# Kernel optimization log

Hardware: AMD Instinct MI355X
Metric: run time of the kernel (lower is better)

The kernel has to match this reference:

```python
import jax, jax.numpy as jnp
import numpy as np

DIM_D = 32
DIM_J = 32
DIM_X = 2 * DIM_D + 1  # 65: (dim_d+1) vd slice + dim_d C_R slice
DIM_H = 256
N = 100
DT = 0.01
JUMP_P = 0.05  # per-step jump probability
BATCH = 4096


def setup_inputs() -> dict:
    key = jax.random.key(0)
    ks = jax.random.split(key, 8)

    def he(k, shape):  # kaiming_normal_, fan_in mode (matches torch init)
        return (jax.random.normal(k, shape, dtype=jnp.float32)
                * jnp.sqrt(2.0 / shape[1]))

    W1 = he(ks[0], (DIM_H, DIM_X + 1))
    W2 = he(ks[1], (DIM_H, DIM_H))
    W3 = he(ks[2], (DIM_H, DIM_H))
    W4 = he(ks[3], (DIM_D, DIM_H))
    b1 = jnp.zeros((DIM_H,), jnp.float32)
    b2 = jnp.zeros((DIM_H,), jnp.float32)
    b3 = jnp.zeros((DIM_H,), jnp.float32)
    b4 = jnp.zeros((DIM_D,), jnp.float32)
    # x_0 in (0, 0.5) so -log(1 - x) is well defined; s, d positive rates
    x_0 = jax.random.uniform(ks[4], (DIM_X,), jnp.float32, 0.05, 0.5)
    s = jax.random.uniform(ks[5], (DIM_D, 1), jnp.float32, 0.5, 1.5)
    d_param = jax.random.uniform(ks[6], (1,), jnp.float32, 0.5, 1.5)
    return {"W1": W1, "b1": b1, "W2": W2, "b2": b2, "W3": W3, "b3": b3,
            "W4": W4, "b4": b4, "x_0": x_0, "s": s, "d_param": d_param,
            "batch_size": BATCH}


def _forward(W1, b1, W2, b2, W3, b3, W4, b4, x_0, s, d_param, batch_size):
    B = batch_size

    def phi(z):  # 4-layer MLP: relu x3 -> sigmoid, control in (0,1)^dim_d
        z = jax.nn.relu(z @ W1.T + b1)
        z = jax.nn.relu(z @ W2.T + b2)
        z = jax.nn.relu(z @ W3.T + b3)
        return jax.nn.sigmoid(z @ W4.T + b4)

    x0 = jnp.broadcast_to(x_0.astype(jnp.float32), (B, DIM_X))
    h_V0 = -jnp.log(1.0 - x0[:, :DIM_D]) / s[:, 0]          # [B, D]
    h_D0 = x0[:, DIM_D:DIM_D + 1] / d_param[0]              # [B, 1]
    h0 = jnp.concatenate([h_V0, h_D0], axis=-1)             # [B, D+1]
    CR0 = x0[:, -DIM_D:]                                    # [B, D]
    f0 = jnp.zeros((B, 1), jnp.float32)
    base_key = jax.random.key(1234)

    def step(carry, n):
        x, h, C_R, f = carry
        t = DT * n.astype(jnp.float32)
        time = jnp.ones((B, 1), jnp.float32) * t
        control = phi(jnp.concatenate([x, time], axis=-1))  # [B, D]
        k = jax.random.fold_in(base_key, n)
        jumps = jax.random.bernoulli(k, JUMP_P, (B, DIM_J)).astype(jnp.float32)
        # running cost f += f(t, x) * dt
        f = f + jnp.sum(x[:, :DIM_D], axis=-1, keepdims=True) * DT
        # step_forward: hazard clocks advance by dt, jump resets V-clocks
        hV = jnp.where(jumps > 0, 0.0, h[:, :DIM_D] + DT)
        hD = h[:, DIM_D:] + DT
        h_new = jnp.concatenate([hV, hD], axis=-1)
        # dCR: cumulative reward driven by control at jump times
        C_R_new = C_R + control * jumps
        # h_to_vd: invert the h_V / h_D maps
        V = 1.0 - jnp.exp(-s[:, 0] * hV)                     # [B, D]
        Dv = d_param[0] * hD                                 # [B, 1]
        x_new = jnp.concatenate([V, Dv, C_R_new], axis=-1)   # [B, 2D+1]
        return (x_new, h_new, C_R_new, f), (control, x_new)

    (x_last, _, _, f), (controls, xs) = jax.lax.scan(
        step, (x0, h0, CR0, f0), jnp.arange(N - 1))
    # control_tensor[:, n] filled for n < N-1, last row stays zero (as in torch)
    control_tensor = jnp.concatenate(
        [jnp.swapaxes(controls, 0, 1), jnp.zeros((B, 1, DIM_D), jnp.float32)],
        axis=1)                                              # [B, N, D]
    x_tensor = jnp.concatenate(
        [x0[:, None, :], jnp.swapaxes(xs, 0, 1)], axis=1)    # [B, N, 2D+1]
    # J = f + g(x, poiss); g = terminal value of cumulative reward slice
    J = f + jnp.sum(x_last[:, -DIM_D:], axis=-1, keepdims=True)
    return control_tensor, x_tensor, J[:, :, None]


def reference(W1, b1, W2, b2, W3, b3, W4, b4, x_0, s, d_param, batch_size):
    return _forward(W1, b1, W2, b2, W3, b3, W4, b4, x_0, s, d_param,
                    int(batch_size))
```

## Files before the change

kernel.cpp:

```cpp
#include <hip/hip_runtime.h>
#include <cstdint>
#include <cstddef>

#define DIM_D 32
#define KIN   66
#define DIM_H 256
#define NSTE  100
#define BATCHN 4096
#define ROWS  16
#define BLKT  512
#define NBLK  (BATCHN / ROWS)

#define CTRL_OFF 0
#define X_OFF ((size_t)BATCHN * NSTE * DIM_D)
#define J_OFF (X_OFF + (size_t)BATCHN * NSTE * 65)

#define W1B_OFF 0
#define W2B_OFF 24576
#define W3B_OFF 90112
#define W4B_OFF 155648
#define WS_ELEMS 163840

constexpr float DT_C = 0.01f;

typedef __bf16 bf16x8 __attribute__((ext_vector_type(8)));
typedef float  f32x4  __attribute__((ext_vector_type(4)));

__device__ __forceinline__ uint32_t rotl32(uint32_t x, int n) {
  return (x << n) | (x >> (32 - n));
}

__device__ __forceinline__ void tf2x32(uint32_t k0, uint32_t k1,
                                       uint32_t x0, uint32_t x1,
                                       uint32_t& o0, uint32_t& o1) {
  uint32_t k2 = k0 ^ k1 ^ 0x1BD11BDAu;
#define TFR(r) { x0 += x1; x1 = rotl32(x1, (r)); x1 ^= x0; }
  x0 += k0; x1 += k1;
  TFR(13) TFR(15) TFR(26) TFR(6)   x0 += k1; x1 += k2 + 1u;
  TFR(17) TFR(29) TFR(16) TFR(24)  x0 += k2; x1 += k0 + 2u;
  TFR(13) TFR(15) TFR(26) TFR(6)   x0 += k0; x1 += k1 + 3u;
  TFR(17) TFR(29) TFR(16) TFR(24)  x0 += k1; x1 += k2 + 4u;
  TFR(13) TFR(15) TFR(26) TFR(6)   x0 += k2; x1 += k0 + 5u;
#undef TFR
  o0 = x0; o1 = x1;
}

__global__ void conv_w(const float* __restrict__ W1, const float* __restrict__ W2,
                       const float* __restrict__ W3, const float* __restrict__ W4,
                       __bf16* __restrict__ ws) {
  int t = blockIdx.x * 256 + threadIdx.x;
  if (t < W2B_OFF) {
    int r = t / 96, c = t % 96;
    ws[t] = (c < KIN) ? (__bf16)W1[r * KIN + c] : (__bf16)0.0f;
  } else if (t < W3B_OFF) {
    ws[t] = (__bf16)W2[t - W2B_OFF];
  } else if (t < W4B_OFF) {
    ws[t] = (__bf16)W3[t - W3B_OFF];
  } else if (t < WS_ELEMS) {
    ws[t] = (__bf16)W4[t - W4B_OFF];
  }
}

__device__ __forceinline__ f32x4 mfma16(bf16x8 a, bf16x8 b, f32x4 c) {
  return __builtin_amdgcn_mfma_f32_16x16x32_bf16(a, b, c, 0, 0, 0);
}

__device__ __forceinline__ int swz256(int row, int col) { return row * 256 + (col ^ ((row & 15) << 4)); }
__device__ __forceinline__ int swz512(int row, int col) { return row * 512 + (col ^ ((row & 15) << 4)); }

__global__ void __launch_bounds__(BLKT)
__attribute__((amdgpu_waves_per_eu(2, 2))) model_kernel(
    const __bf16* __restrict__ ws,
    const float* __restrict__ b1, const float* __restrict__ b2,
    const float* __restrict__ b3, const float* __restrict__ b4,
    const float* __restrict__ x0p, const float* __restrict__ sp,
    const float* __restrict__ dpp, float* __restrict__ out)
{
  __shared__ __bf16 xb[16 * 128];
  __shared__ __bf16 zA[16 * 256];
  __shared__ __bf16 zB[16 * 256];
  __shared__ __bf16 scr[8 * 16 * 40];
  __shared__ float  psum[8][16][32];
  __shared__ uint32_t keys[NSTE - 1][2];
  __shared__ uint32_t jb[NSTE - 1][16];

  const int tid = threadIdx.x;
  const int r0  = blockIdx.x * ROWS;
  char* xbB = (char*)xb;
  char* zAB = (char*)zA;
  char* zBB = (char*)zB;

  const int wv  = tid >> 6;
  const int ln  = tid & 63;
  const int lr  = ln & 15;
  const int g   = ln >> 4;
  const int lk8 = g * 8;
  const int er  = tid >> 5, ed = tid & 31;

  if (tid < NSTE - 1) {
    uint32_t o0, o1;
    tf2x32(0u, 1234u, 0u, (uint32_t)tid, o0, o1);
    keys[tid][0] = o0; keys[tid][1] = o1;
  }
  for (int i = tid; i < 16 * 128; i += BLKT) xb[i] = (__bf16)0.0f;
  const float dp = dpp[0];
  __syncthreads();

  {
    const int rr = 2 * wv + (ln >> 5);
    const int dd = ln & 31;
    const uint32_t F = (uint32_t)((r0 + rr) * DIM_D + dd);
    for (int n = 0; n < NSTE - 1; ++n) {
      uint32_t o0, o1;
      tf2x32(keys[n][0], keys[n][1], 0u, F, o0, o1);
      const uint32_t bits = o0 ^ o1;
      const float uf = __uint_as_float((bits >> 9) | 0x3f800000u) - 1.0f;
      const unsigned long long m = __ballot(uf < 0.05f);
      if (ln == 0)       jb[n][rr] = (uint32_t)m;
      else if (ln == 32) jb[n][rr] = (uint32_t)(m >> 32);
    }
  }

  float V, cr, hv, vsum = 0.f, hD = 0.f, s_d, b4d;
  size_t ctrlb, xbase;
  {
    s_d = sp[ed];
    b4d = b4[ed];
    V  = x0p[ed];
    cr = x0p[33 + ed];
    hv = -logf(1.0f - V) / s_d;
    ctrlb = CTRL_OFF + (size_t)(r0 + er) * NSTE * DIM_D;
    xbase = X_OFF + (size_t)(r0 + er) * NSTE * 65;
    *(__bf16*)(xbB + swz256(er, ed * 2))        = (__bf16)V;
    *(__bf16*)(xbB + swz256(er, (33 + ed) * 2)) = (__bf16)cr;
    out[xbase + ed] = V;
    out[xbase + 33 + ed] = cr;
    out[ctrlb + (size_t)(NSTE - 1) * DIM_D + ed] = 0.0f;
    if (ed == 0) {
      hD = x0p[DIM_D] / dp;
      *(__bf16*)(xbB + swz256(er, 64))  = (__bf16)x0p[DIM_D];
      *(__bf16*)(xbB + swz256(er, 130)) = (__bf16)0.0f;
      out[xbase + 32] = x0p[DIM_D];
    }
  }

  bf16x8 w1f[2][3], w2f[2][8], w3f[2][8], w4t[2];
#pragma unroll
  for (int t = 0; t < 2; ++t) {
    const int n1c = wv * 32 + t * 16 + lr;
#pragma unroll
    for (int ks = 0; ks < 3; ++ks)
      w1f[t][ks] = *(const bf16x8*)(ws + W1B_OFF + n1c * 96 + ks * 32 + lk8);
#pragma unroll
    for (int ks = 0; ks < 8; ++ks) {
      w2f[t][ks] = *(const bf16x8*)(ws + W2B_OFF + n1c * 256 + ks * 32 + lk8);
      w3f[t][ks] = *(const bf16x8*)(ws + W3B_OFF + n1c * 256 + ks * 32 + lk8);
    }
    w4t[t] = *(const bf16x8*)(ws + W4B_OFF + (t * 16 + lr) * 256 + wv * 32 + lk8);
  }
  const float bb1_0 = b1[wv * 32 + lr], bb1_1 = b1[wv * 32 + 16 + lr];
  const float bb2_0 = b2[wv * 32 + lr], bb2_1 = b2[wv * 32 + 16 + lr];
  const float bb3_0 = b3[wv * 32 + lr], bb3_1 = b3[wv * 32 + 16 + lr];
  __syncthreads();

  float u_s = 0.f, V_s = 0.f, cr_s = 0.f, Dv_s = 0.f;

  for (int n = 0; n < NSTE - 1; ++n) {
    if (n > 0) {
      out[ctrlb + (size_t)(n - 1) * DIM_D + ed] = u_s;
      const size_t xo = xbase + (size_t)n * 65;
      out[xo + ed] = V_s;
      out[xo + 33 + ed] = cr_s;
      if (ed == 0) out[xo + 32] = Dv_s;
    }

    {
      f32x4 a0 = {bb1_0, bb1_0, bb1_0, bb1_0};
      f32x4 a1 = {bb1_1, bb1_1, bb1_1, bb1_1};
      f32x4 a0o = {0, 0, 0, 0}, a1o = {0, 0, 0, 0};
      bf16x8 af0 = *(const bf16x8*)(xbB + swz256(lr, g * 16));
      bf16x8 af1 = *(const bf16x8*)(xbB + swz256(lr, 64 + g * 16));
      bf16x8 af2 = *(const bf16x8*)(xbB + swz256(lr, 128 + g * 16));
      a0  = mfma16(af0, w1f[0][0], a0);  a1  = mfma16(af0, w1f[1][0], a1);
      a0o = mfma16(af1, w1f[0][1], a0o); a1o = mfma16(af1, w1f[1][1], a1o);
      a0  = mfma16(af2, w1f[0][2], a0);  a1  = mfma16(af2, w1f[1][2], a1);
      a0 += a0o; a1 += a1o;
#pragma unroll
      for (int q = 0; q < 4; ++q) {
        const int row = g * 4 + q;
        *(__bf16*)(zAB + swz512(row, (wv * 32 + lr) * 2))      = (__bf16)fmaxf(a0[q], 0.0f);
        *(__bf16*)(zAB + swz512(row, (wv * 32 + 16 + lr) * 2)) = (__bf16)fmaxf(a1[q], 0.0f);
      }
    }
    __syncthreads();

    {
      f32x4 a0 = {bb2_0, bb2_0, bb2_0, bb2_0};
      f32x4 a1 = {bb2_1, bb2_1, bb2_1, bb2_1};
      f32x4 a0o = {0, 0, 0, 0}, a1o = {0, 0, 0, 0};
#pragma unroll
      for (int ks = 0; ks < 8; ks += 2) {
        bf16x8 afe = *(const bf16x8*)(zAB + swz512(lr, ks * 64 + g * 16));
        a0  = mfma16(afe, w2f[0][ks], a0);
        a1  = mfma16(afe, w2f[1][ks], a1);
        bf16x8 afo = *(const bf16x8*)(zAB + swz512(lr, (ks + 1) * 64 + g * 16));
        a0o = mfma16(afo, w2f[0][ks + 1], a0o);
        a1o = mfma16(afo, w2f[1][ks + 1], a1o);
      }
      a0 += a0o; a1 += a1o;
#pragma unroll
      for (int q = 0; q < 4; ++q) {
        const int row = g * 4 + q;
        *(__bf16*)(zBB + swz512(row, (wv * 32 + lr) * 2))      = (__bf16)fmaxf(a0[q], 0.0f);
        *(__bf16*)(zBB + swz512(row, (wv * 32 + 16 + lr) * 2)) = (__bf16)fmaxf(a1[q], 0.0f);
      }
    }
    __syncthreads();

    {
      f32x4 a0 = {bb3_0, bb3_0, bb3_0, bb3_0};
      f32x4 a1 = {bb3_1, bb3_1, bb3_1, bb3_1};
      f32x4 a0o = {0, 0, 0, 0}, a1o = {0, 0, 0, 0};
#pragma unroll
      for (int ks = 0; ks < 8; ks += 2) {
        bf16x8 afe = *(const bf16x8*)(zBB + swz512(lr, ks * 64 + g * 16));
        a0  = mfma16(afe, w3f[0][ks], a0);
        a1  = mfma16(afe, w3f[1][ks], a1);
        bf16x8 afo = *(const bf16x8*)(zBB + swz512(lr, (ks + 1) * 64 + g * 16));
        a0o = mfma16(afo, w3f[0][ks + 1], a0o);
        a1o = mfma16(afo, w3f[1][ks + 1], a1o);
      }
      a0 += a0o; a1 += a1o;
      char* sw = (char*)scr + wv * 1280;
#pragma unroll
      for (int q = 0; q < 4; ++q) {
        const int row = g * 4 + q;
        *(__bf16*)(sw + row * 80 + lr * 2)      = (__bf16)fmaxf(a0[q], 0.0f);
        *(__bf16*)(sw + row * 80 + 32 + lr * 2) = (__bf16)fmaxf(a1[q], 0.0f);
      }
      asm volatile("s_waitcnt lgkmcnt(0)" ::: "memory");
      const bf16x8 a4 = *(const bf16x8*)(sw + lr * 80 + g * 16);
      f32x4 c0 = {0, 0, 0, 0}, c1 = {0, 0, 0, 0};
      c0 = mfma16(a4, w4t[0], c0);
      c1 = mfma16(a4, w4t[1], c1);
#pragma unroll
      for (int q = 0; q < 4; ++q) {
        psum[wv][g * 4 + q][lr]      = c0[q];
        psum[wv][g * 4 + q][16 + lr] = c1[q];
      }
    }
    __syncthreads();

    {
      vsum += V;
      float up = b4d;
#pragma unroll
      for (int w = 0; w < 8; ++w) up += psum[w][er][ed];
      const float u = 1.0f / (1.0f + __expf(-up));
      const bool jump = (jb[n][er] >> ed) & 1;
      hv = jump ? 0.0f : (hv + DT_C);
      cr += jump ? u : 0.0f;
      V = 1.0f - __expf(-s_d * hv);
      *(__bf16*)(xbB + swz256(er, ed * 2))        = (__bf16)V;
      *(__bf16*)(xbB + swz256(er, (33 + ed) * 2)) = (__bf16)cr;
      if (ed == 0) {
        hD += DT_C;
        Dv_s = dp * hD;
        *(__bf16*)(xbB + swz256(er, 64))  = (__bf16)Dv_s;
        *(__bf16*)(xbB + swz256(er, 130)) = (__bf16)(DT_C * (float)(n + 1));
      }
      u_s = u; V_s = V; cr_s = cr;
    }
    __syncthreads();
  }

  {
    out[ctrlb + (size_t)(NSTE - 2) * DIM_D + ed] = u_s;
    const size_t xo = xbase + (size_t)(NSTE - 1) * 65;
    out[xo + ed] = V_s;
    out[xo + 33 + ed] = cr_s;
    if (ed == 0) out[xo + 32] = Dv_s;

    float c = cr, vv = vsum;
#pragma unroll
    for (int m = 1; m < 32; m <<= 1) {
      c  += __shfl_xor(c,  m, 32);
      vv += __shfl_xor(vv, m, 32);
    }
    if (ed == 0) out[J_OFF + (size_t)(r0 + er)] = DT_C * vv + c;
  }
}

extern "C" void kernel_launch(void* const* d_in, const int* in_sizes, int n_in,
                              void* d_out, int out_size, void* d_ws, size_t ws_size,
                              hipStream_t stream) {
  const float* W1 = (const float*)d_in[0];
  const float* b1 = (const float*)d_in[1];
  const float* W2 = (const float*)d_in[2];
  const float* b2 = (const float*)d_in[3];
  const float* W3 = (const float*)d_in[4];
  const float* b3 = (const float*)d_in[5];
  const float* W4 = (const float*)d_in[6];
  const float* b4 = (const float*)d_in[7];
  const float* x0 = (const float*)d_in[8];
  const float* s  = (const float*)d_in[9];
  const float* dp = (const float*)d_in[10];
  __bf16* ws = (__bf16*)d_ws;
  float* out = (float*)d_out;

  hipLaunchKernelGGL(conv_w, dim3(WS_ELEMS / 256), dim3(256), 0, stream, W1, W2, W3, W4, ws);
  hipLaunchKernelGGL(model_kernel, dim3(NBLK), dim3(BLKT), 0, stream,
                     ws, b1, b2, b3, b4, x0, s, dp, out);
}
```

Before: 306.9 us.

## Double block to 16 waves, each wave owning 16 hidden columns

```diff
diff --git a/kernel.cpp b/kernel.cpp
--- a/kernel.cpp
+++ b/kernel.cpp
@@ -4,11 +4,10 @@
 
 #define DIM_D 32
 #define KIN   66
-#define DIM_H 256
 #define NSTE  100
 #define BATCHN 4096
 #define ROWS  16
-#define BLKT  512
+#define BLKT  1024
 #define NBLK  (BATCHN / ROWS)
 
 #define CTRL_OFF 0
@@ -51,7 +50,7 @@
   int t = blockIdx.x * 256 + threadIdx.x;
   if (t < W2B_OFF) {
     int r = t / 96, c = t % 96;
-    ws[t] = (c < KIN) ? (__bf16)W1[r * KIN + c] : (__bf16)0.0f;
+    ws[t] = (c < KIN) ? (__bf16)W1[r * 66 + c] : (__bf16)0.0f;
   } else if (t < W3B_OFF) {
     ws[t] = (__bf16)W2[t - W2B_OFF];
   } else if (t < W4B_OFF) {
@@ -68,8 +67,7 @@
 __device__ __forceinline__ int swz256(int row, int col) { return row * 256 + (col ^ ((row & 15) << 4)); }
 __device__ __forceinline__ int swz512(int row, int col) { return row * 512 + (col ^ ((row & 15) << 4)); }
 
-__global__ void __launch_bounds__(BLKT)
-__attribute__((amdgpu_waves_per_eu(2, 2))) model_kernel(
+__global__ void __launch_bounds__(BLKT, 4) model_kernel(
     const __bf16* __restrict__ ws,
     const float* __restrict__ b1, const float* __restrict__ b2,
     const float* __restrict__ b3, const float* __restrict__ b4,
@@ -79,8 +77,8 @@
   __shared__ __bf16 xb[16 * 128];
   __shared__ __bf16 zA[16 * 256];
   __shared__ __bf16 zB[16 * 256];
-  __shared__ __bf16 scr[8 * 16 * 40];
-  __shared__ float  psum[8][16][32];
+  __shared__ __bf16 scr[16 * 320];
+  __shared__ __bf16 psum[16 * 32 * 16];
   __shared__ uint32_t keys[NSTE - 1][2];
   __shared__ uint32_t jb[NSTE - 1][16];
 
@@ -89,12 +87,14 @@
   char* xbB = (char*)xb;
   char* zAB = (char*)zA;
   char* zBB = (char*)zB;
+  char* psB = (char*)psum;
 
   const int wv  = tid >> 6;
   const int ln  = tid & 63;
   const int lr  = ln & 15;
   const int g   = ln >> 4;
   const int lk8 = g * 8;
+  const int hc  = wv * 16 + lr;
   const int er  = tid >> 5, ed = tid & 31;
 
   if (tid < NSTE - 1) {
@@ -107,10 +107,12 @@
   __syncthreads();
 
   {
-    const int rr = 2 * wv + (ln >> 5);
+    const int rr = 2 * (wv & 7) + (ln >> 5);
     const int dd = ln & 31;
     const uint32_t F = (uint32_t)((r0 + rr) * DIM_D + dd);
-    for (int n = 0; n < NSTE - 1; ++n) {
+    const int n0 = (wv >> 3) * 50;
+    const int n1 = (wv >> 3) ? (NSTE - 1) : 50;
+    for (int n = n0; n < n1; ++n) {
       uint32_t o0, o1;
       tf2x32(keys[n][0], keys[n][1], 0u, F, o0, o1);
       const uint32_t bits = o0 ^ o1;
@@ -121,9 +123,10 @@
     }
   }
 
-  float V, cr, hv, vsum = 0.f, hD = 0.f, s_d, b4d;
-  size_t ctrlb, xbase;
-  {
+  float V = 0.f, cr = 0.f, hv = 0.f, vsum = 0.f, hD = 0.f;
+  float s_d = 1.f, b4d = 0.f;
+  size_t ctrlb = 0, xbase = 0;
+  if (tid < 512) {
     s_d = sp[ed];
     b4d = b4[ed];
     V  = x0p[ed];
@@ -144,29 +147,31 @@
     }
   }
 
-  bf16x8 w1f[2][3], w2f[2][8], w3f[2][8], w4t[2];
-#pragma unroll
-  for (int t = 0; t < 2; ++t) {
-    const int n1c = wv * 32 + t * 16 + lr;
-#pragma unroll
-    for (int ks = 0; ks < 3; ++ks)
-      w1f[t][ks] = *(const bf16x8*)(ws + W1B_OFF + n1c * 96 + ks * 32 + lk8);
-#pragma unroll
-    for (int ks = 0; ks < 8; ++ks) {
-      w2f[t][ks] = *(const bf16x8*)(ws + W2B_OFF + n1c * 256 + ks * 32 + lk8);
-      w3f[t][ks] = *(const bf16x8*)(ws + W3B_OFF + n1c * 256 + ks * 32 + lk8);
-    }
-    w4t[t] = *(const bf16x8*)(ws + W4B_OFF + (t * 16 + lr) * 256 + wv * 32 + lk8);
-  }
-  const float bb1_0 = b1[wv * 32 + lr], bb1_1 = b1[wv * 32 + 16 + lr];
-  const float bb2_0 = b2[wv * 32 + lr], bb2_1 = b2[wv * 32 + 16 + lr];
-  const float bb3_0 = b3[wv * 32 + lr], bb3_1 = b3[wv * 32 + 16 + lr];
+  bf16x8 w1f[3], w2f[8], w3f[8], w4t[2];
+#pragma unroll
+  for (int ks = 0; ks < 3; ++ks)
+    w1f[ks] = *(const bf16x8*)(ws + W1B_OFF + hc * 96 + ks * 32 + lk8);
+#pragma unroll
+  for (int ks = 0; ks < 8; ++ks) {
+    w2f[ks] = *(const bf16x8*)(ws + W2B_OFF + hc * 256 + ks * 32 + lk8);
+    w3f[ks] = *(const bf16x8*)(ws + W3B_OFF + hc * 256 + ks * 32 + lk8);
+  }
+  {
+    const bf16x8 z8 = bf16x8{};
+#pragma unroll
+    for (int t = 0; t < 2; ++t)
+      w4t[t] = (g < 2) ? *(const bf16x8*)(ws + W4B_OFF + (t * 16 + lr) * 256 + wv * 16 + g * 8)
+                       : z8;
+  }
+  const float bb1 = b1[hc];
+  const float bb2 = b2[hc];
+  const float bb3 = b3[hc];
   __syncthreads();
 
   float u_s = 0.f, V_s = 0.f, cr_s = 0.f, Dv_s = 0.f;
 
   for (int n = 0; n < NSTE - 1; ++n) {
-    if (n > 0) {
+    if (n > 0 && tid < 512) {
       out[ctrlb + (size_t)(n - 1) * DIM_D + ed] = u_s;
       const size_t xo = xbase + (size_t)n * 65;
       out[xo + ed] = V_s;
@@ -175,87 +180,64 @@
     }
 
     {
-      f32x4 a0 = {bb1_0, bb1_0, bb1_0, bb1_0};
-      f32x4 a1 = {bb1_1, bb1_1, bb1_1, bb1_1};
-      f32x4 a0o = {0, 0, 0, 0}, a1o = {0, 0, 0, 0};
+      f32x4 a0 = {bb1, bb1, bb1, bb1};
       bf16x8 af0 = *(const bf16x8*)(xbB + swz256(lr, g * 16));
       bf16x8 af1 = *(const bf16x8*)(xbB + swz256(lr, 64 + g * 16));
       bf16x8 af2 = *(const bf16x8*)(xbB + swz256(lr, 128 + g * 16));
-      a0  = mfma16(af0, w1f[0][0], a0);  a1  = mfma16(af0, w1f[1][0], a1);
-      a0o = mfma16(af1, w1f[0][1], a0o); a1o = mfma16(af1, w1f[1][1], a1o);
-      a0  = mfma16(af2, w1f[0][2], a0);  a1  = mfma16(af2, w1f[1][2], a1);
-      a0 += a0o; a1 += a1o;
-#pragma unroll
-      for (int q = 0; q < 4; ++q) {
-        const int row = g * 4 + q;
-        *(__bf16*)(zAB + swz512(row, (wv * 32 + lr) * 2))      = (__bf16)fmaxf(a0[q], 0.0f);
-        *(__bf16*)(zAB + swz512(row, (wv * 32 + 16 + lr) * 2)) = (__bf16)fmaxf(a1[q], 0.0f);
-      }
+      a0 = mfma16(af0, w1f[0], a0);
+      a0 = mfma16(af1, w1f[1], a0);
+      a0 = mfma16(af2, w1f[2], a0);
+#pragma unroll
+      for (int q = 0; q < 4; ++q)
+        *(__bf16*)(zAB + swz512(g * 4 + q, hc * 2)) = (__bf16)fmaxf(a0[q], 0.0f);
     }
     __syncthreads();
 
     {
-      f32x4 a0 = {bb2_0, bb2_0, bb2_0, bb2_0};
-      f32x4 a1 = {bb2_1, bb2_1, bb2_1, bb2_1};
-      f32x4 a0o = {0, 0, 0, 0}, a1o = {0, 0, 0, 0};
-#pragma unroll
-      for (int ks = 0; ks < 8; ks += 2) {
-        bf16x8 afe = *(const bf16x8*)(zAB + swz512(lr, ks * 64 + g * 16));
-        a0  = mfma16(afe, w2f[0][ks], a0);
-        a1  = mfma16(afe, w2f[1][ks], a1);
-        bf16x8 afo = *(const bf16x8*)(zAB + swz512(lr, (ks + 1) * 64 + g * 16));
-        a0o = mfma16(afo, w2f[0][ks + 1], a0o);
-        a1o = mfma16(afo, w2f[1][ks + 1], a1o);
-      }
-      a0 += a0o; a1 += a1o;
-#pragma unroll
-      for (int q = 0; q < 4; ++q) {
-        const int row = g * 4 + q;
-        *(__bf16*)(zBB + swz512(row, (wv * 32 + lr) * 2))      = (__bf16)fmaxf(a0[q], 0.0f);
-        *(__bf16*)(zBB + swz512(row, (wv * 32 + 16 + lr) * 2)) = (__bf16)fmaxf(a1[q], 0.0f);
-      }
+      f32x4 a0 = {bb2, bb2, bb2, bb2};
+#pragma unroll
+      for (int ks = 0; ks < 8; ++ks) {
+        bf16x8 af = *(const bf16x8*)(zAB + swz512(lr, ks * 64 + g * 16));
+        a0 = mfma16(af, w2f[ks], a0);
+      }
+#pragma unroll
+      for (int q = 0; q < 4; ++q)
+        *(__bf16*)(zBB + swz512(g * 4 + q, hc * 2)) = (__bf16)fmaxf(a0[q], 0.0f);
     }
     __syncthreads();
 
     {
-      f32x4 a0 = {bb3_0, bb3_0, bb3_0, bb3_0};
-      f32x4 a1 = {bb3_1, bb3_1, bb3_1, bb3_1};
-      f32x4 a0o = {0, 0, 0, 0}, a1o = {0, 0, 0, 0};
-#pragma unroll
-      for (int ks = 0; ks < 8; ks += 2) {
-        bf16x8 afe = *(const bf16x8*)(zBB + swz512(lr, ks * 64 + g * 16));
-        a0  = mfma16(afe, w3f[0][ks], a0);
-        a1  = mfma16(afe, w3f[1][ks], a1);
-        bf16x8 afo = *(const bf16x8*)(zBB + swz512(lr, (ks + 1) * 64 + g * 16));
-        a0o = mfma16(afo, w3f[0][ks + 1], a0o);
-        a1o = mfma16(afo, w3f[1][ks + 1], a1o);
-      }
-      a0 += a0o; a1 += a1o;
-      char* sw = (char*)scr + wv * 1280;
-#pragma unroll
-      for (int q = 0; q < 4; ++q) {
-        const int row = g * 4 + q;
-        *(__bf16*)(sw + row * 80 + lr * 2)      = (__bf16)fmaxf(a0[q], 0.0f);
-        *(__bf16*)(sw + row * 80 + 32 + lr * 2) = (__bf16)fmaxf(a1[q], 0.0f);
-      }
+      f32x4 a0 = {bb3, bb3, bb3, bb3};
+#pragma unroll
+      for (int ks = 0; ks < 8; ++ks) {
+        bf16x8 af = *(const bf16x8*)(zBB + swz512(lr, ks * 64 + g * 16));
+        a0 = mfma16(af, w3f[ks], a0);
+      }
+      char* sw = (char*)scr + wv * 640;
+#pragma unroll
+      for (int q = 0; q < 4; ++q)
+        *(__bf16*)(sw + (g * 4 + q) * 40 + lr * 2) = (__bf16)fmaxf(a0[q], 0.0f);
       asm volatile("s_waitcnt lgkmcnt(0)" ::: "memory");
-      const bf16x8 a4 = *(const bf16x8*)(sw + lr * 80 + g * 16);
+      bf16x8 a4 = bf16x8{};
+      if (g < 2) a4 = *(const bf16x8*)(sw + lr * 40 + g * 16);
       f32x4 c0 = {0, 0, 0, 0}, c1 = {0, 0, 0, 0};
       c0 = mfma16(a4, w4t[0], c0);
       c1 = mfma16(a4, w4t[1], c1);
 #pragma unroll
       for (int q = 0; q < 4; ++q) {
-        psum[wv][g * 4 + q][lr]      = c0[q];
-        psum[wv][g * 4 + q][16 + lr] = c1[q];
-      }
-    }
-    __syncthreads();
-
-    {
+        *(__bf16*)(psB + (g * 4 + q) * 1024 + lr * 32 + wv * 2)        = (__bf16)c0[q];
+        *(__bf16*)(psB + (g * 4 + q) * 1024 + (16 + lr) * 32 + wv * 2) = (__bf16)c1[q];
+      }
+    }
+    __syncthreads();
+
+    if (tid < 512) {
       vsum += V;
       float up = b4d;
-#pragma unroll
-      for (int w = 0; w < 8; ++w) up += psum[w][er][ed];
+      const bf16x8 p0 = *(const bf16x8*)(psB + er * 1024 + ed * 32);
+      const bf16x8 p1 = *(const bf16x8*)(psB + er * 1024 + ed * 32 + 16);
+#pragma unroll
+      for (int i = 0; i < 8; ++i) up += (float)p0[i] + (float)p1[i];
       const float u = 1.0f / (1.0f + __expf(-up));
       const bool jump = (jb[n][er] >> ed) & 1;
       hv = jump ? 0.0f : (hv + DT_C);
@@ -274,7 +256,7 @@
     __syncthreads();
   }
 
-  {
+  if (tid < 512) {
     out[ctrlb + (size_t)(NSTE - 2) * DIM_D + ed] = u_s;
     const size_t xo = xbase + (size_t)(NSTE - 1) * 65;
     out[xo + ed] = V_s;
```

New measurement: 819.1 us. +166.9%, slower.
